# Kernel tuning notes

Hardware: AMD Instinct MI355X
Metric: run time of the kernel (lower is better)

## Reference

```python
import jax, jax.numpy as jnp
import numpy as np

MAX_DISP = 4  # matches init_kwargs


def setup_inputs() -> dict:
    key = jax.random.key(0)
    k1, k2 = jax.random.split(key)
    fmap1 = jax.random.normal(k1, (8, 256, 64, 128), dtype=jnp.float32)
    fmap2 = jax.random.normal(k2, (8, 256, 64, 128), dtype=jnp.float32)
    return {"fmap1": fmap1, "fmap2": fmap2}


def reference(fmap1, fmap2):
    # corr(x,y,dx,dy) = sum_c fmap1[c,y,x] * fmap2[c,y+dy,x+dx]
    pad = MAX_DISP
    B, C, H, W = fmap1.shape
    f2p = jnp.pad(fmap2, ((0, 0), (0, 0), (pad, pad), (pad, pad)))
    side = 2 * pad + 1  # 9 -> 81 displacements total
    # Loop over the small fixed set of 81 static displacements; each term is a
    # fused elementwise-multiply + channel reduction (einsum over c).
    corrs = [
        jnp.einsum('bchw,bchw->bhw', fmap1, f2p[:, :, y0:y0 + H, x0:x0 + W])
        for y0 in range(side)
        for x0 in range(side)
    ]
    return jnp.stack(corrs, axis=1)  # (B, 81, H, W)
```

## Files before the change

kernel.cpp:

```cpp
#include <hip/hip_runtime.h>


namespace {
constexpr int B_ = 8, C_ = 256, H_ = 64, W_ = 128;
constexpr int SIDE = 9, ND = 81, PAD = 4;
constexpr int HW = H_ * W_;
constexpr int KC = 32, NCH = C_ / KC;
constexpr int YB = 8, RWS = YB + 2 * PAD;
constexpr int XB = 16;
constexpr int NQ = 4;
constexpr int YP_ = H_ + 2 * PAD;
constexpr int XP_ = 144;
constexpr size_t ROWU = (size_t)NQ * XP_;
constexpr size_t PERB = (size_t)NCH * YP_ * ROWU;
constexpr size_t NW2 = (size_t)B_ * PERB;
constexpr size_t WS_BYTES = NW2 * 16;
constexpr int TILE_U4 = RWS * NQ * 32;
constexpr int EPS_SLOTS = ND * YB * XB / 4;
}

typedef __attribute__((ext_vector_type(8))) short short8;
typedef __attribute__((ext_vector_type(4))) float float4v;
typedef __attribute__((address_space(1))) void gvoid;
typedef __attribute__((address_space(3))) void svoid;

__device__ __forceinline__ unsigned bf16rne(float f) {
  unsigned u = __float_as_uint(f);
  return (u + 0x7fffu + ((u >> 16) & 1u)) >> 16;
}
__device__ __forceinline__ unsigned packbf2(float lo, float hi) {
  return bf16rne(lo) | (bf16rne(hi) << 16);
}

__global__ __launch_bounds__(256)
void cvt_f2(const float* __restrict__ f2, uint4* __restrict__ w2) {
  const int id = blockIdx.x;
  const int b = id & 7;
  const int e2 = (id >> 3) * 256 + (int)threadIdx.x;
  const int xp2 = e2 % (XP_ / 2);
  int r = e2 / (XP_ / 2);
  const int q = r & 3;
  r >>= 2;
  const int yp = r % YP_;
  const int cs = r / YP_;
  const int xp = 2 * xp2;
  const int yg = yp - PAD, xg = xp - PAD;
  uint4 o0 = {0u, 0u, 0u, 0u}, o1 = o0;
  if (yg >= 0 && yg < H_ && xg >= 0 && xg <= W_ - 2) {
    const float* s =
        f2 + ((size_t)(b * C_ + cs * KC + q * 8) * H_ + yg) * W_ + xg;
    const float2 v0 = *(const float2*)(s + 0 * HW);
    const float2 v1 = *(const float2*)(s + 1 * HW);
    const float2 v2 = *(const float2*)(s + 2 * HW);
    const float2 v3 = *(const float2*)(s + 3 * HW);
    const float2 v4 = *(const float2*)(s + 4 * HW);
    const float2 v5 = *(const float2*)(s + 5 * HW);
    const float2 v6 = *(const float2*)(s + 6 * HW);
    const float2 v7 = *(const float2*)(s + 7 * HW);
    o0.x = packbf2(v0.x, v1.x);  o1.x = packbf2(v0.y, v1.y);
    o0.y = packbf2(v2.x, v3.x);  o1.y = packbf2(v2.y, v3.y);
    o0.z = packbf2(v4.x, v5.x);  o1.z = packbf2(v4.y, v5.y);
    o0.w = packbf2(v6.x, v7.x);  o1.w = packbf2(v6.y, v7.y);
  }
  const size_t e = (((size_t)(cs * YP_ + yp) * NQ + q) * XP_) + xp;
  uint4* d = w2 + (size_t)b * PERB + e;
  d[0] = o0;
  d[1] = o1;
}

__global__ __launch_bounds__(512, 4)
void corr_mfma2(const float* __restrict__ f1, const uint4* __restrict__ w2,
                float* __restrict__ out) {
  __shared__ uint4 f2s[2 * TILE_U4];

  const int id = blockIdx.x;
  const int b = id & 7;
  const int k = id >> 3;
  const int xg = k & 7, yg = k >> 3;
  const int x0 = xg * XB, y0 = yg * YB;

  const int t = threadIdx.x, lane = t & 63, w = t >> 6;
  const int v = lane & 15, q = lane >> 4;
  const int sq = q << 1;
  const int l_hi = lane >> 5;
  const int l_xq = lane & 31;

  const uint4* w2b = w2 + (size_t)b * PERB;
  const float* f1b = f1 + (size_t)b * C_ * HW;

  auto issue_stage = [&](int ch, int buf) {
    const uint4* wc = w2b + (size_t)ch * ((size_t)YP_ * ROWU);
#pragma unroll
    for (int kk = 0; kk < 4; ++kk) {
      const int r = 2 * w + (kk >> 1);
      const int qp = kk & 1;
      const int qq = 2 * qp + l_hi;
      const int xqs = l_xq ^ (qq << 1);
      const uint4* gp = wc + (size_t)(y0 + r) * ROWU + (size_t)qq * XP_ + x0 + xqs;
      uint4* lp = &f2s[buf * TILE_U4 + (r * NQ + qp * 2) * 32];
      __builtin_amdgcn_global_load_lds((gvoid*)gp, (svoid*)lp, 16, 0, 0);
    }
  };
  auto issue_f1 = [&](int ch, float* p) {
    const float* fp =
        f1b + ((size_t)(ch * KC + q * 8) * H_ + (y0 + w)) * W_ + x0 + v;
#pragma unroll
    for (int j = 0; j < 8; ++j) p[j] = fp[(size_t)j * HW];
  };

  float4v acc[SIDE][2];
#pragma unroll
  for (int i = 0; i < SIDE; ++i) {
    acc[i][0] = (float4v){0.f, 0.f, 0.f, 0.f};
    acc[i][1] = (float4v){0.f, 0.f, 0.f, 0.f};
  }

  float p0[8], p1[8];
  issue_stage(0, 0);
  __builtin_amdgcn_sched_barrier(0);
  issue_f1(0, p0);
  __builtin_amdgcn_sched_barrier(0);
  issue_stage(1, 1);
  __builtin_amdgcn_sched_barrier(0);

#pragma unroll
  for (int ch = 0; ch < NCH; ++ch) {
    float* pc = (ch & 1) ? p1 : p0;
    uint4 afu;
    afu.x = packbf2(pc[0], pc[1]);
    afu.y = packbf2(pc[2], pc[3]);
    afu.z = packbf2(pc[4], pc[5]);
    afu.w = packbf2(pc[6], pc[7]);
    const short8 af = __builtin_bit_cast(short8, afu);

    asm volatile("s_waitcnt vmcnt(4)" ::: "memory");
    __builtin_amdgcn_s_barrier();
    __builtin_amdgcn_sched_barrier(0);

    if (ch + 1 < NCH) issue_f1(ch + 1, (ch & 1) ? p0 : p1);

    const int bo = (ch & 1) * TILE_U4;
#pragma unroll
    for (int dy = 0; dy < SIDE; ++dy) {
      const uint4* base = &f2s[bo + ((w + dy) * NQ + q) * 32];
      const short8 b0 = __builtin_bit_cast(short8, base[v ^ sq]);
      const short8 b1 = __builtin_bit_cast(short8, base[(v + 16) ^ sq]);
      acc[dy][0] =
          __builtin_amdgcn_mfma_f32_16x16x32_bf16(af, b0, acc[dy][0], 0, 0, 0);
      acc[dy][1] =
          __builtin_amdgcn_mfma_f32_16x16x32_bf16(af, b1, acc[dy][1], 0, 0, 0);
    }
    __builtin_amdgcn_sched_barrier(0);
    __builtin_amdgcn_s_barrier();
    __builtin_amdgcn_sched_barrier(0);
    if (ch + 2 < NCH) issue_stage(ch + 2, ch & 1);
  }

  __builtin_amdgcn_s_barrier();
  float* eps = (float*)f2s;
#pragma unroll
  for (int dy = 0; dy < SIDE; ++dy) {
#pragma unroll
    for (int r = 0; r < 4; ++r) {
      const int m = q * 4 + r;
      const int dx0 = v - m;
      if (dx0 >= 0 && dx0 <= 8)
        eps[((dy * SIDE + dx0) * YB + w) * XB + m] = acc[dy][0][r];
      const int dx1 = dx0 + 16;
      if (dx1 <= 8)
        eps[((dy * SIDE + dx1) * YB + w) * XB + m] = acc[dy][1][r];
    }
  }
  __builtin_amdgcn_s_barrier();
  float* outp = out + (size_t)b * ND * HW;
  for (int s = t; s < EPS_SLOTS; s += 512) {
    const int p = s >> 5;
    const int yy = (s & 31) >> 2;
    const int xq = s & 3;
    const float4 val = *(const float4*)&eps[s * 4];
    *(float4*)&outp[((size_t)p * H_ + y0 + yy) * W_ + x0 + xq * 4] = val;
  }
}

namespace fb {
constexpr int PXS = 20, F2PX = 32, F2U = 16 * (F2PX / 4) * 16;
}

__global__ __launch_bounds__(512, 4)
void corr_fb(const float* __restrict__ f1, const float* __restrict__ f2,
             float* __restrict__ out) {
  using namespace fb;
  __shared__ __align__(16) unsigned f2s[RWS * F2PX * PXS];
  __shared__ __align__(16) unsigned f1s[YB * XB * PXS];

  const int id = blockIdx.x;
  const int b = id & 7;
  const int k = id >> 3;
  const int xg = k & 7, yg = k >> 3;
  const int x0 = xg * XB, y0 = yg * YB;
  const int t = threadIdx.x, lane = t & 63, w = t >> 6;
  const int v = lane & 15, q = lane >> 4;

  float4v acc[SIDE][2];
#pragma unroll
  for (int i = 0; i < SIDE; ++i) {
    acc[i][0] = (float4v){0.f, 0.f, 0.f, 0.f};
    acc[i][1] = (float4v){0.f, 0.f, 0.f, 0.f};
  }
  const float* __restrict__ f1b = f1 + (size_t)b * C_ * HW;
  const float* __restrict__ f2b = f2 + (size_t)b * C_ * HW;

  for (int ch = 0; ch < NCH; ++ch) {
    const int c0 = ch * KC;
    if (ch) __syncthreads();
#pragma unroll
    for (int u0 = 0; u0 < F2U; u0 += 512) {
      const int u = u0 + t;
      const int cp = u & 15;
      const int t2 = u >> 4;
      const int pxq = t2 & 7;
      const int r = t2 >> 3;
      const int ygl = y0 - PAD + r;
      const int xb = x0 - PAD + pxq * 4;
      float4 va = make_float4(0.f, 0.f, 0.f, 0.f), vb = va;
      if (ygl >= 0 && ygl < H_ && xb >= 0 && xb <= W_ - 4) {
        const float* p = f2b + ((size_t)(c0 + 2 * cp) * H_ + ygl) * W_ + xb;
        va = *(const float4*)p;
        vb = *(const float4*)(p + HW);
      }
      unsigned* d = &f2s[(r * F2PX + pxq * 4) * PXS + cp];
      d[0 * PXS] = packbf2(va.x, vb.x);
      d[1 * PXS] = packbf2(va.y, vb.y);
      d[2 * PXS] = packbf2(va.z, vb.z);
      d[3 * PXS] = packbf2(va.w, vb.w);
    }
    {
      const int cp = t & 15;
      const int t2 = t >> 4;
      const int pxq = t2 & 3;
      const int r = t2 >> 2;
      const float* p =
          f1b + ((size_t)(c0 + 2 * cp) * H_ + (y0 + r)) * W_ + x0 + pxq * 4;
      const float4 va = *(const float4*)p;
      const float4 vb = *(const float4*)(p + HW);
      unsigned* d = &f1s[(r * XB + pxq * 4) * PXS + cp];
      d[0 * PXS] = packbf2(va.x, vb.x);
      d[1 * PXS] = packbf2(va.y, vb.y);
      d[2 * PXS] = packbf2(va.z, vb.z);
      d[3 * PXS] = packbf2(va.w, vb.w);
    }
    __syncthreads();

    const short8 af = __builtin_bit_cast(
        short8, *(const uint4*)&f1s[(w * XB + v) * PXS + 4 * q]);
#pragma unroll
    for (int dy = 0; dy < SIDE; ++dy) {
      const unsigned* fp = &f2s[((w + dy) * F2PX + v) * PXS + 4 * q];
      const short8 b0 = __builtin_bit_cast(short8, *(const uint4*)fp);
      const short8 b1 =
          __builtin_bit_cast(short8, *(const uint4*)(fp + 16 * PXS));
      acc[dy][0] =
          __builtin_amdgcn_mfma_f32_16x16x32_bf16(af, b0, acc[dy][0], 0, 0, 0);
      acc[dy][1] =
          __builtin_amdgcn_mfma_f32_16x16x32_bf16(af, b1, acc[dy][1], 0, 0, 0);
    }
  }
  const int y = y0 + w;
  float* outb = out + (size_t)b * ND * HW + (size_t)y * W_ + x0;
#pragma unroll
  for (int dy = 0; dy < SIDE; ++dy) {
#pragma unroll
    for (int r = 0; r < 4; ++r) {
      const int m = q * 4 + r;
      const int dx0 = v - m;
      if (dx0 >= 0 && dx0 <= 8)
        outb[(size_t)(dy * SIDE + dx0) * HW + m] = acc[dy][0][r];
      const int dx1 = v - m + 16;
      if (dx1 <= 8)
        outb[(size_t)(dy * SIDE + dx1) * HW + m] = acc[dy][1][r];
    }
  }
}

extern "C" void kernel_launch(void* const* d_in, const int* in_sizes, int n_in,
                              void* d_out, int out_size, void* d_ws,
                              size_t ws_size, hipStream_t stream) {
  (void)in_sizes; (void)n_in; (void)out_size;
  const float* f1 = (const float*)d_in[0];
  const float* f2 = (const float*)d_in[1];
  float* out = (float*)d_out;
  if (ws_size >= WS_BYTES) {
    uint4* w2 = (uint4*)d_ws;
    cvt_f2<<<dim3((unsigned)(NW2 / 512)), 256, 0, stream>>>(f2, w2);
    corr_mfma2<<<dim3(512), 512, 0, stream>>>(f1, w2, out);
  } else {
    corr_fb<<<dim3(512), 512, 0, stream>>>(f1, f2, out);
  }
}
```

Baseline: 179.4 us.

## Double row tile per wave to reuse fmap2 LDS rows across two output rows

The MFMA correlation kernel now covers 16 output rows per block instead of 8. Each wave handles two adjacent rows, so each B fragment loaded from LDS feeds MFMAs for both rows through a sliding register window. This cuts LDS reads and the halo overhead per output row, and halves the grid to 256 blocks. In exchange, accumulator and f1 register use doubles and launch bounds drop to 2 blocks per CU, which reduces occupancy and may leave CUs underused with only 256 blocks.

```diff
diff --git a/kernel.cpp b/kernel.cpp
--- a/kernel.cpp
+++ b/kernel.cpp
@@ -6,7 +6,7 @@
 constexpr int SIDE = 9, ND = 81, PAD = 4;
 constexpr int HW = H_ * W_;
 constexpr int KC = 32, NCH = C_ / KC;
-constexpr int YB = 8, RWS = YB + 2 * PAD;
+constexpr int YB = 16, RWS = YB + 2 * PAD;
 constexpr int XB = 16;
 constexpr int NQ = 4;
 constexpr int YP_ = H_ + 2 * PAD;
@@ -68,8 +68,8 @@
   d[1] = o1;
 }
 
-__global__ __launch_bounds__(512, 4)
-void corr_mfma2(const float* __restrict__ f1, const uint4* __restrict__ w2,
+__global__ __launch_bounds__(512, 2)
+void corr_mfma5(const float* __restrict__ f1, const uint4* __restrict__ w2,
                 float* __restrict__ out) {
   __shared__ uint4 f2s[2 * TILE_U4];
 
@@ -91,31 +91,36 @@
   auto issue_stage = [&](int ch, int buf) {
     const uint4* wc = w2b + (size_t)ch * ((size_t)YP_ * ROWU);
 #pragma unroll
-    for (int kk = 0; kk < 4; ++kk) {
-      const int r = 2 * w + (kk >> 1);
-      const int qp = kk & 1;
+    for (int kk = 0; kk < 6; ++kk) {
+      const int g = w * 6 + kk;
+      const int r = g >> 1, qp = g & 1;
       const int qq = 2 * qp + l_hi;
       const int xqs = l_xq ^ (qq << 1);
-      const uint4* gp = wc + (size_t)(y0 + r) * ROWU + (size_t)qq * XP_ + x0 + xqs;
+      const uint4* gp =
+          wc + (size_t)(y0 + r) * ROWU + (size_t)qq * XP_ + x0 + xqs;
       uint4* lp = &f2s[buf * TILE_U4 + (r * NQ + qp * 2) * 32];
       __builtin_amdgcn_global_load_lds((gvoid*)gp, (svoid*)lp, 16, 0, 0);
     }
   };
   auto issue_f1 = [&](int ch, float* p) {
     const float* fp =
-        f1b + ((size_t)(ch * KC + q * 8) * H_ + (y0 + w)) * W_ + x0 + v;
+        f1b + ((size_t)(ch * KC + q * 8) * H_ + (y0 + 2 * w)) * W_ + x0 + v;
 #pragma unroll
     for (int j = 0; j < 8; ++j) p[j] = fp[(size_t)j * HW];
+#pragma unroll
+    for (int j = 0; j < 8; ++j) p[8 + j] = fp[(size_t)j * HW + W_];
   };
 
-  float4v acc[SIDE][2];
-#pragma unroll
-  for (int i = 0; i < SIDE; ++i) {
-    acc[i][0] = (float4v){0.f, 0.f, 0.f, 0.f};
-    acc[i][1] = (float4v){0.f, 0.f, 0.f, 0.f};
-  }
-
-  float p0[8], p1[8];
+  float4v acc[2][SIDE][2];
+#pragma unroll
+  for (int i = 0; i < 2; ++i)
+#pragma unroll
+    for (int d = 0; d < SIDE; ++d) {
+      acc[i][d][0] = (float4v){0.f, 0.f, 0.f, 0.f};
+      acc[i][d][1] = (float4v){0.f, 0.f, 0.f, 0.f};
+    }
+
+  float p0[16], p1[16];
   issue_stage(0, 0);
   __builtin_amdgcn_sched_barrier(0);
   issue_f1(0, p0);
@@ -126,29 +131,51 @@
 #pragma unroll
   for (int ch = 0; ch < NCH; ++ch) {
     float* pc = (ch & 1) ? p1 : p0;
-    uint4 afu;
-    afu.x = packbf2(pc[0], pc[1]);
-    afu.y = packbf2(pc[2], pc[3]);
-    afu.z = packbf2(pc[4], pc[5]);
-    afu.w = packbf2(pc[6], pc[7]);
-    const short8 af = __builtin_bit_cast(short8, afu);
-
-    asm volatile("s_waitcnt vmcnt(4)" ::: "memory");
+    uint4 a0u, a1u;
+    a0u.x = packbf2(pc[0], pc[1]);
+    a0u.y = packbf2(pc[2], pc[3]);
+    a0u.z = packbf2(pc[4], pc[5]);
+    a0u.w = packbf2(pc[6], pc[7]);
+    a1u.x = packbf2(pc[8], pc[9]);
+    a1u.y = packbf2(pc[10], pc[11]);
+    a1u.z = packbf2(pc[12], pc[13]);
+    a1u.w = packbf2(pc[14], pc[15]);
+    const short8 af0 = __builtin_bit_cast(short8, a0u);
+    const short8 af1 = __builtin_bit_cast(short8, a1u);
+
+    asm volatile("s_waitcnt vmcnt(6)" ::: "memory");
     __builtin_amdgcn_s_barrier();
     __builtin_amdgcn_sched_barrier(0);
 
     if (ch + 1 < NCH) issue_f1(ch + 1, (ch & 1) ? p0 : p1);
 
     const int bo = (ch & 1) * TILE_U4;
+    uint4 bA0, bA1, bB0, bB1;
+    {
+      const uint4* ra = &f2s[bo + ((2 * w) * NQ + q) * 32];
+      bA0 = ra[v ^ sq];
+      bA1 = ra[(v + 16) ^ sq];
+      const uint4* rb = &f2s[bo + ((2 * w + 1) * NQ + q) * 32];
+      bB0 = rb[v ^ sq];
+      bB1 = rb[(v + 16) ^ sq];
+    }
 #pragma unroll
     for (int dy = 0; dy < SIDE; ++dy) {
-      const uint4* base = &f2s[bo + ((w + dy) * NQ + q) * 32];
-      const short8 b0 = __builtin_bit_cast(short8, base[v ^ sq]);
-      const short8 b1 = __builtin_bit_cast(short8, base[(v + 16) ^ sq]);
-      acc[dy][0] =
-          __builtin_amdgcn_mfma_f32_16x16x32_bf16(af, b0, acc[dy][0], 0, 0, 0);
-      acc[dy][1] =
-          __builtin_amdgcn_mfma_f32_16x16x32_bf16(af, b1, acc[dy][1], 0, 0, 0);
+      if (dy > 0) {
+        bA0 = bB0;
+        bA1 = bB1;
+        const uint4* rb = &f2s[bo + ((2 * w + 1 + dy) * NQ + q) * 32];
+        bB0 = rb[v ^ sq];
+        bB1 = rb[(v + 16) ^ sq];
+      }
+      acc[0][dy][0] = __builtin_amdgcn_mfma_f32_16x16x32_bf16(
+          af0, __builtin_bit_cast(short8, bA0), acc[0][dy][0], 0, 0, 0);
+      acc[0][dy][1] = __builtin_amdgcn_mfma_f32_16x16x32_bf16(
+          af0, __builtin_bit_cast(short8, bA1), acc[0][dy][1], 0, 0, 0);
+      acc[1][dy][0] = __builtin_amdgcn_mfma_f32_16x16x32_bf16(
+          af1, __builtin_bit_cast(short8, bB0), acc[1][dy][0], 0, 0, 0);
+      acc[1][dy][1] = __builtin_amdgcn_mfma_f32_16x16x32_bf16(
+          af1, __builtin_bit_cast(short8, bB1), acc[1][dy][1], 0, 0, 0);
     }
     __builtin_amdgcn_sched_barrier(0);
     __builtin_amdgcn_s_barrier();
@@ -159,23 +186,26 @@
   __builtin_amdgcn_s_barrier();
   float* eps = (float*)f2s;
 #pragma unroll
-  for (int dy = 0; dy < SIDE; ++dy) {
-#pragma unroll
-    for (int r = 0; r < 4; ++r) {
-      const int m = q * 4 + r;
-      const int dx0 = v - m;
-      if (dx0 >= 0 && dx0 <= 8)
-        eps[((dy * SIDE + dx0) * YB + w) * XB + m] = acc[dy][0][r];
-      const int dx1 = dx0 + 16;
-      if (dx1 <= 8)
-        eps[((dy * SIDE + dx1) * YB + w) * XB + m] = acc[dy][1][r];
+  for (int i = 0; i < 2; ++i) {
+#pragma unroll
+    for (int dy = 0; dy < SIDE; ++dy) {
+#pragma unroll
+      for (int r = 0; r < 4; ++r) {
+        const int m = q * 4 + r;
+        const int dx0 = v - m;
+        if (dx0 >= 0 && dx0 <= 8)
+          eps[((dy * SIDE + dx0) * YB + 2 * w + i) * XB + m] = acc[i][dy][0][r];
+        const int dx1 = dx0 + 16;
+        if (dx1 <= 8)
+          eps[((dy * SIDE + dx1) * YB + 2 * w + i) * XB + m] = acc[i][dy][1][r];
+      }
     }
   }
   __builtin_amdgcn_s_barrier();
   float* outp = out + (size_t)b * ND * HW;
   for (int s = t; s < EPS_SLOTS; s += 512) {
-    const int p = s >> 5;
-    const int yy = (s & 31) >> 2;
+    const int p = s >> 6;
+    const int yy = (s & 63) >> 2;
     const int xq = s & 3;
     const float4 val = *(const float4*)&eps[s * 4];
     *(float4*)&outp[((size_t)p * H_ + y0 + yy) * W_ + x0 + xq * 4] = val;
@@ -183,21 +213,22 @@
 }
 
 namespace fb {
-constexpr int PXS = 20, F2PX = 32, F2U = 16 * (F2PX / 4) * 16;
+constexpr int PXS = 20, F2PX = 32, RWSf = 16, YBf = 8;
+constexpr int F2U = RWSf * (F2PX / 4) * 16;
 }
 
 __global__ __launch_bounds__(512, 4)
 void corr_fb(const float* __restrict__ f1, const float* __restrict__ f2,
              float* __restrict__ out) {
   using namespace fb;
-  __shared__ __align__(16) unsigned f2s[RWS * F2PX * PXS];
-  __shared__ __align__(16) unsigned f1s[YB * XB * PXS];
+  __shared__ __align__(16) unsigned f2s[RWSf * F2PX * PXS];
+  __shared__ __align__(16) unsigned f1s[YBf * XB * PXS];
 
   const int id = blockIdx.x;
   const int b = id & 7;
   const int k = id >> 3;
   const int xg = k & 7, yg = k >> 3;
-  const int x0 = xg * XB, y0 = yg * YB;
+  const int x0 = xg * XB, y0 = yg * YBf;
   const int t = threadIdx.x, lane = t & 63, w = t >> 6;
   const int v = lane & 15, q = lane >> 4;
 
@@ -292,7 +323,7 @@
   if (ws_size >= WS_BYTES) {
     uint4* w2 = (uint4*)d_ws;
     cvt_f2<<<dim3((unsigned)(NW2 / 512)), 256, 0, stream>>>(f2, w2);
-    corr_mfma2<<<dim3(512), 512, 0, stream>>>(f1, w2, out);
+    corr_mfma5<<<dim3(256), 512, 0, stream>>>(f1, w2, out);
   } else {
     corr_fb<<<dim3(512), 512, 0, stream>>>(f1, f2, out);
   }
```

After: 175.8 us. -2.0%, faster.
